# Optimization experiments

Hardware: AMD Instinct MI355X
Metric: run time of the kernel (lower is better)

## Reference

```python
import jax, jax.numpy as jnp
from jax import lax
import numpy as np

WIDTH = 3.0        # tool half-width (voxels)
SIGMA = 1.0        # soft mask edge (voxels)
BLUR_SIGMA = 1.5   # post-deposit isotropic blur sigma (voxels)
EPS = 1e-8


def _gauss_blur(x, sigma):
    """Separable Gaussian blur over the last two axes of x: [B, X, Y]."""
    radius = int(3 * sigma)
    t = jnp.arange(-radius, radius + 1, dtype=x.dtype)
    k = jnp.exp(-0.5 * (t / sigma) ** 2)
    k = k / k.sum()
    x4 = x[:, None]                      # [B,1,X,Y] NCHW
    kh = k.reshape(1, 1, -1, 1)
    x4 = lax.conv_general_dilated(x4, kh, (1, 1), 'SAME')
    kw = k.reshape(1, 1, 1, -1)
    x4 = lax.conv_general_dilated(x4, kw, (1, 1), 'SAME')
    return x4[:, 0]


def setup_inputs() -> dict:
    key = jax.random.key(0)
    k1, k2, k3 = jax.random.split(key, 3)
    B, H, W = 16, 1024, 1024
    occ = jax.random.uniform(k1, (B, H, W), dtype=jnp.float32)
    # push start/end points well inside the grid (voxel coordinates)
    action_start = jax.random.uniform(k2, (B, 3), minval=200.0, maxval=800.0, dtype=jnp.float32)
    action_end = action_start + jax.random.uniform(k3, (B, 3), minval=-150.0, maxval=150.0, dtype=jnp.float32)
    return {"occ": occ, "action_start": action_start, "action_end": action_end}


def reference(occ, action_start, action_end):
    # coordinate-convention transpose (see SplatPushModel docs)
    rho = jnp.swapaxes(occ, 1, 2)            # [B, X, Y]
    B, X, Y = rho.shape
    p0 = action_start[:, :2]                 # [B,2]
    p1 = action_end[:, :2]                   # [B,2]

    d = p1 - p0
    L = jnp.sqrt(jnp.sum(d * d, axis=-1) + EPS)      # [B] segment length
    u = d / L[:, None]                               # unit push direction
    n = jnp.stack([-u[:, 1], u[:, 0]], axis=-1)      # unit normal

    gx = jnp.arange(X, dtype=rho.dtype)[None, :, None]   # [1,X,1]
    gy = jnp.arange(Y, dtype=rho.dtype)[None, None, :]   # [1,1,Y]
    bc = lambda v: v[:, None, None]                      # [B] -> [B,1,1]

    # --- swept band: soft distance-to-segment mask ---
    rx = gx - bc(p0[:, 0])
    ry = gy - bc(p0[:, 1])
    t = jnp.clip(rx * bc(u[:, 0]) + ry * bc(u[:, 1]), 0.0, L[:, None, None])
    dx = rx - t * bc(u[:, 0])
    dy = ry - t * bc(u[:, 1])
    dist = jnp.sqrt(dx * dx + dy * dy + EPS)
    swept = jax.nn.sigmoid((WIDTH - dist) / SIGMA)       # [B,X,Y]

    m_swept = jnp.sum(rho * swept, axis=(1, 2))          # [B] mass to move
    pile_depth = m_swept / (2.0 * WIDTH)                 # [B]

    # --- landing zone probe (rectangle past p1) ---
    qx = gx - bc(p1[:, 0])
    qy = gy - bc(p1[:, 1])
    s = qx * bc(u[:, 0]) + qy * bc(u[:, 1])              # along-direction coord
    r = qx * bc(n[:, 0]) + qy * bc(n[:, 1])              # perpendicular coord
    lat = jax.nn.sigmoid((WIDTH - jnp.abs(r)) / SIGMA)
    probe = jax.nn.sigmoid(s / SIGMA) * jax.nn.sigmoid((bc(pile_depth) - s) / SIGMA) * lat
    existing = jnp.sum(rho * probe, axis=(1, 2))         # [B]
    extra = existing / (2.0 * WIDTH)                     # [B] forward extension

    # --- deposit band, shifted forward by extra_depth ---
    dep_mask = (jax.nn.sigmoid((s - bc(extra)) / SIGMA)
                * jax.nn.sigmoid((bc(extra) + bc(pile_depth) - s) / SIGMA)
                * lat)
    dep_norm = m_swept / (jnp.sum(dep_mask, axis=(1, 2)) + EPS)
    dep = dep_mask * dep_norm[:, None, None]             # mass-conserving deposit

    if BLUR_SIGMA > 0:
        dep = _gauss_blur(dep, BLUR_SIGMA)

    rho_new = rho * (1.0 - swept) + dep
    return jnp.swapaxes(rho_new, 1, 2)
```

## Files before the change

kernel.cpp:

```cpp
#include <hip/hip_runtime.h>
#include <math.h>

#define BB    16
#define HH    1024
#define WW    1024
#define EPSF  1e-8f
#define RAD   4
#define MARG  24.f
#define NB1   128
#define NB3   32
#define WMAX  128
#define FW    (WMAX + 16)
#define UNR   4

struct BlurK { float k[9]; };

__device__ __forceinline__ float sigf(float z) {
    z = fmaxf(fminf(z, 40.f), -40.f);
    return 1.f / (1.f + __expf(-z));
}

struct Geom { float p0x, p0y, p1x, p1y, L, ux, uy; };

__device__ __forceinline__ Geom load_geom(const float* as, const float* ae, int b) {
    Geom g;
    g.p0x = as[3 * b];  g.p0y = as[3 * b + 1];
    g.p1x = ae[3 * b];  g.p1y = ae[3 * b + 1];
    float dx = g.p1x - g.p0x, dy = g.p1y - g.p0y;
    g.L  = sqrtf(dx * dx + dy * dy + EPSF);
    g.ux = dx / g.L;  g.uy = dy / g.L;
    return g;
}

__device__ __forceinline__ float sweptf(const Geom& g, float x, float y) {
    float rx = x - g.p0x, ry = y - g.p0y;
    float t  = fminf(fmaxf(rx * g.ux + ry * g.uy, 0.f), g.L);
    float dx = rx - t * g.ux, dy = ry - t * g.uy;
    float dist = sqrtf(dx * dx + dy * dy + EPSF);
    return sigf(3.f - dist);
}

__device__ __forceinline__ void slat(const Geom& g, float x, float y, float& s, float& lat) {
    float qx = x - g.p1x, qy = y - g.p1y;
    s = qx * g.ux + qy * g.uy;
    float r = qx * (-g.uy) + qy * g.ux;
    lat = sigf(3.f - fabsf(r));
}

__device__ __forceinline__ void capsule_bbox(const Geom& g, float m,
                                             int& x0, int& x1, int& y0, int& y1) {
    x0 = max(0, (int)floorf(fminf(g.p0x, g.p1x) - m));
    x1 = min(WW - 1, (int)ceilf(fmaxf(g.p0x, g.p1x) + m));
    y0 = max(0, (int)floorf(fminf(g.p0y, g.p1y) - m));
    y1 = min(HH - 1, (int)ceilf(fmaxf(g.p0y, g.p1y) + m));
}

__device__ __forceinline__ void strip_bbox(const Geom& g, float s0, float s1, float m,
                                           int& x0, int& x1, int& y0, int& y1) {
    float xmin = 1e9f, xmax = -1e9f, ymin = 1e9f, ymax = -1e9f;
    #pragma unroll
    for (int i = 0; i < 4; i++) {
        float s = (i & 1) ? s1 : s0;
        float r = (i & 2) ? m : -m;
        float x = g.p1x + s * g.ux - r * g.uy;
        float y = g.p1y + s * g.uy + r * g.ux;
        xmin = fminf(xmin, x); xmax = fmaxf(xmax, x);
        ymin = fminf(ymin, y); ymax = fmaxf(ymax, y);
    }
    x0 = max(0, (int)floorf(xmin)); x1 = min(WW - 1, (int)ceilf(xmax));
    y0 = max(0, (int)floorf(ymin)); y1 = min(HH - 1, (int)ceilf(ymax));
}

__device__ __forceinline__ bool ivx(float a, float A, float B, float& lo, float& hi) {
    if (fabsf(a) < 1e-5f) return !(A > 0.f || B < 0.f);
    float l = A / a, h = B / a;
    if (a < 0.f) { float t = l; l = h; h = t; }
    lo = fmaxf(lo, l); hi = fminf(hi, h);
    return true;
}

__device__ __forceinline__ float brb256(float v, float* sm) {
    #pragma unroll
    for (int off = 32; off > 0; off >>= 1) v += __shfl_down(v, off);
    const int lane = threadIdx.x & 63, wid = threadIdx.x >> 6;
    if (lane == 0) sm[wid] = v;
    __syncthreads();
    float r = sm[0] + sm[1] + sm[2] + sm[3];
    __syncthreads();
    return r;
}

__device__ __forceinline__ float brb1024(float v, float* sm) {
    #pragma unroll
    for (int off = 32; off > 0; off >>= 1) v += __shfl_down(v, off);
    const int lane = threadIdx.x & 63, wid = threadIdx.x >> 6;
    if (lane == 0) sm[wid] = v;
    __syncthreads();
    float r = 0.f;
    #pragma unroll
    for (int i = 0; i < 16; i++) r += sm[i];
    __syncthreads();
    return r;
}

__global__ __launch_bounds__(256)
void k_main(const float* __restrict__ occ, const float* __restrict__ as,
            const float* __restrict__ ae, float* __restrict__ out,
            float* __restrict__ part1) {
    const int b = blockIdx.y, bx = blockIdx.x, tid = threadIdx.x;
    Geom g = load_geom(as, ae, b);
    const size_t ibase = (size_t)b << 20;
    const float4* src = (const float4*)(occ + ibase);
    float4*       dst = (float4*)(out + ibase);
    const int yb = bx * 8;
    const int base4 = bx * 2048 + tid;

    float4 v[8];
    #pragma unroll
    for (int k = 0; k < 8; k++) v[k] = src[base4 + k * 256];

    int cx0, cx1, cy0, cy1; capsule_bbox(g, MARG, cx0, cx1, cy0, cy1);
    const int x = tid << 2;
    float msum = 0.f;
    if (x + 3 >= cx0 && x <= cx1) {
        #pragma unroll
        for (int k = 0; k < 8; k++) {
            const int y = yb + k;
            if (y >= cy0 && y <= cy1) {
                const float fy = (float)y, fx = (float)x;
                const float s0 = sweptf(g, fx + 0.f, fy);
                const float s1 = sweptf(g, fx + 1.f, fy);
                const float s2 = sweptf(g, fx + 2.f, fy);
                const float s3 = sweptf(g, fx + 3.f, fy);
                msum += v[k].x * s0 + v[k].y * s1 + v[k].z * s2 + v[k].w * s3;
                v[k].x *= 1.f - s0; v[k].y *= 1.f - s1;
                v[k].z *= 1.f - s2; v[k].w *= 1.f - s3;
            }
        }
    }
    #pragma unroll
    for (int k = 0; k < 8; k++) dst[base4 + k * 256] = v[k];

    __shared__ float sm[4];
    const float bs = brb256(msum, sm);
    if (tid == 0) part1[b * NB1 + bx] = bs;
}

__global__ __launch_bounds__(1024)
void k_probe(const float* __restrict__ occ, const float* __restrict__ as,
             const float* __restrict__ ae, const float* __restrict__ part1,
             float* __restrict__ sc) {
    const int b = blockIdx.x, tid = threadIdx.x;
    const int tx4 = tid & 63;
    const int ty  = tid >> 6;
    __shared__ float sm[16];
    Geom g = load_geom(as, ae, b);
    const float4* src4 = (const float4*)(occ + ((size_t)b << 20));

    const float m_swept = brb1024((tid < NB1) ? part1[b * NB1 + tid] : 0.f, sm);
    const float pile = m_swept * (1.f / 6.f);

    int x0, x1, y0, y1;
    strip_bbox(g, -MARG, pile + MARG, MARG, x0, x1, y0, y1);
    int c0 = x0 >> 2, c1 = x1 >> 2;
    float sum = 0.f;
    for (int cc = c0; cc <= c1; cc += 64) {
        const int c = cc + tx4;
        const bool cok = (c <= c1);
        const float fx = (float)(c << 2);
        for (int y = y0 + ty; y <= y1; y += 16 * UNR) {
            float4 vv[UNR];
            #pragma unroll
            for (int j = 0; j < UNR; j++) {
                const int yy = y + 16 * j;
                vv[j] = (cok && yy <= y1) ? src4[yy * 256 + c]
                                          : make_float4(0.f, 0.f, 0.f, 0.f);
            }
            #pragma unroll
            for (int j = 0; j < UNR; j++) {
                const int yy = y + 16 * j;
                if (cok && yy <= y1) {
                    const float fy = (float)yy;
                    #pragma unroll
                    for (int e = 0; e < 4; e++) {
                        float s, lat; slat(g, fx + (float)e, fy, s, lat);
                        sum += (&vv[j].x)[e] * sigf(s) * sigf(pile - s) * lat;
                    }
                }
            }
        }
    }
    const float existing = brb1024(sum, sm);
    const float extra = existing * (1.f / 6.f);

    strip_bbox(g, extra - MARG, extra + pile + MARG, MARG, x0, x1, y0, y1);
    sum = 0.f;
    {
        const int tx = tid & 127, ty8 = tid >> 7;
        for (int y = y0 + ty8; y <= y1; y += 8) {
            const float fy = (float)y;
            for (int x = x0 + tx; x <= x1; x += 128) {
                float s, lat; slat(g, (float)x, fy, s, lat);
                sum += sigf(s - extra) * sigf(extra + pile - s) * lat;
            }
        }
    }
    const float summask = brb1024(sum, sm);

    if (tid == 0) {
        sc[b * 4 + 0] = pile;
        sc[b * 4 + 1] = extra;
        sc[b * 4 + 2] = m_swept / (summask + EPSF);
    }
}

__global__ __launch_bounds__(256)
void k_dep(const float* __restrict__ as, const float* __restrict__ ae,
           const float* __restrict__ sc, float* __restrict__ out, BlurK wk) {
    const int b = blockIdx.y, bx = blockIdx.x, tid = threadIdx.x;
    const float pile     = sc[b * 4 + 0];
    const float extra    = sc[b * 4 + 1];
    const float dep_norm = sc[b * 4 + 2];
    Geom g = load_geom(as, ae, b);

    int sx0, sx1, sy0, sy1;
    strip_bbox(g, extra - MARG, extra + pile + MARG, MARG, sx0, sx1, sy0, sy1);
    if (sx0 > sx1 || sy0 > sy1) return;
    float* outb = out + ((size_t)b << 20);

    __shared__ float draw[16][FW];
    __shared__ float hb[16][WMAX];

    const int nty = (sy1 - sy0) / 8 + 1;
    const float sA = extra - MARG, sB = extra + pile + MARG;

    for (int ty = bx; ty < nty; ty += NB3) {
        const int yt = sy0 + ty * 8;

        float xlo = 1e9f, xhi = -1e9f;
        #pragma unroll
        for (int r = 0; r < 16; r++) {
            const float dy = (float)(yt - RAD + r) - g.p1y;
            float lo = -1e9f, hi = 1e9f;
            bool ok = ivx(g.ux, sA - dy * g.uy, sB - dy * g.uy, lo, hi);
            ok = ok && ivx(-g.uy, -MARG - dy * g.ux, MARG - dy * g.ux, lo, hi);
            if (ok && lo <= hi) { xlo = fminf(xlo, lo); xhi = fmaxf(xhi, hi); }
        }
        const int csx0 = max(sx0, (int)floorf(xlo + g.p1x));
        const int csx1 = min(sx1, (int)ceilf(xhi + g.p1x));
        if (csx0 > csx1) continue;

        for (int cx = csx0 & ~3; cx <= csx1; cx += WMAX) {
            const int w = min(WMAX, csx1 - cx + 1);

            for (int i = tid; i < 16 * FW; i += 256) {
                const int ly = i / FW, lx = i - ly * FW;
                if (lx < w + 8) {
                    const int gy = yt - RAD + ly, gx = cx - RAD + lx;
                    float val = 0.f;
                    if ((unsigned)gx < WW && (unsigned)gy < HH) {
                        float s, lat; slat(g, (float)gx, (float)gy, s, lat);
                        val = sigf(s - extra) * sigf(extra + pile - s) * lat * dep_norm;
                    }
                    draw[ly][lx] = val;
                }
            }
            __syncthreads();

            for (int i = tid; i < 16 * WMAX; i += 256) {
                const int ly = i >> 7, lx = i & 127;
                if (lx < w) {
                    float acc = 0.f;
                    #pragma unroll
                    for (int j = 0; j < 9; j++) acc += wk.k[j] * draw[ly][lx + j];
                    hb[ly][lx] = acc;
                }
            }
            __syncthreads();

            for (int i = tid; i < 8 * WMAX; i += 256) {
                const int k = i >> 7, lx = i & 127;
                if (lx < w) {
                    float acc = 0.f;
                    #pragma unroll
                    for (int j = 0; j < 9; j++) acc += wk.k[j] * hb[k + j][lx];
                    draw[k][lx] = acc;
                }
            }
            __syncthreads();

            for (int i = tid; i < 8 * WMAX; i += 256) {
                const int k = i >> 7, lx = i & 127;
                const int gy = yt + k, gx = cx + lx;
                if (lx < w && (unsigned)gy < HH && (unsigned)gx < WW)
                    outb[((size_t)gy << 10) + gx] += draw[k][lx];
            }
            __syncthreads();
        }
    }
}

extern "C" void kernel_launch(void* const* d_in, const int* in_sizes, int n_in,
                              void* d_out, int out_size, void* d_ws, size_t ws_size,
                              hipStream_t stream) {
    const float* occ = (const float*)d_in[0];
    const float* as  = (const float*)d_in[1];
    const float* ae  = (const float*)d_in[2];
    float* out   = (float*)d_out;
    float* part1 = (float*)d_ws;
    float* sc    = part1 + BB * NB1;

    BlurK wk;
    {
        float s = 0.f;
        for (int i = 0; i < 9; i++) {
            float t = (float)(i - RAD) / 1.5f;
            wk.k[i] = expf(-0.5f * t * t);
            s += wk.k[i];
        }
        for (int i = 0; i < 9; i++) wk.k[i] /= s;
    }

    k_main <<<dim3(NB1, BB), 256,  0, stream>>>(occ, as, ae, out, part1);
    k_probe<<<dim3(BB),      1024, 0, stream>>>(occ, as, ae, part1, sc);
    k_dep  <<<dim3(NB3, BB), 256,  0, stream>>>(as, ae, sc, out, wk);
}
```

Measured before the change: 158.8 us.

## Split per-batch probe kernel into multi-block existing and summask reductions

```diff
diff --git a/kernel.cpp b/kernel.cpp
--- a/kernel.cpp
+++ b/kernel.cpp
@@ -8,10 +8,10 @@
 #define RAD   4
 #define MARG  24.f
 #define NB1   128
+#define NB2   64
 #define NB3   32
 #define WMAX  128
 #define FW    (WMAX + 16)
-#define UNR   4
 
 struct BlurK { float k[9]; };
 
@@ -86,19 +86,6 @@
     if (lane == 0) sm[wid] = v;
     __syncthreads();
     float r = sm[0] + sm[1] + sm[2] + sm[3];
-    __syncthreads();
-    return r;
-}
-
-__device__ __forceinline__ float brb1024(float v, float* sm) {
-    #pragma unroll
-    for (int off = 32; off > 0; off >>= 1) v += __shfl_down(v, off);
-    const int lane = threadIdx.x & 63, wid = threadIdx.x >> 6;
-    if (lane == 0) sm[wid] = v;
-    __syncthreads();
-    float r = 0.f;
-    #pragma unroll
-    for (int i = 0; i < 16; i++) r += sm[i];
     __syncthreads();
     return r;
 }
@@ -146,83 +133,70 @@
     if (tid == 0) part1[b * NB1 + bx] = bs;
 }
 
-__global__ __launch_bounds__(1024)
-void k_probe(const float* __restrict__ occ, const float* __restrict__ as,
-             const float* __restrict__ ae, const float* __restrict__ part1,
-             float* __restrict__ sc) {
-    const int b = blockIdx.x, tid = threadIdx.x;
-    const int tx4 = tid & 63;
-    const int ty  = tid >> 6;
-    __shared__ float sm[16];
+__global__ __launch_bounds__(256)
+void k_existing(const float* __restrict__ occ, const float* __restrict__ as,
+                const float* __restrict__ ae, const float* __restrict__ part1,
+                float* __restrict__ part2) {
+    const int b = blockIdx.y, bx = blockIdx.x, tid = threadIdx.x;
+    __shared__ float sm[4];
+    const float m_swept = brb256((tid < NB1) ? part1[b * NB1 + tid] : 0.f, sm);
+    const float pile = m_swept * (1.f / 6.f);
+
     Geom g = load_geom(as, ae, b);
-    const float4* src4 = (const float4*)(occ + ((size_t)b << 20));
-
-    const float m_swept = brb1024((tid < NB1) ? part1[b * NB1 + tid] : 0.f, sm);
-    const float pile = m_swept * (1.f / 6.f);
-
+    int x0, x1, y0, y1; strip_bbox(g, -MARG, pile + MARG, MARG, x0, x1, y0, y1);
+    const float* base = occ + ((size_t)b << 20);
+    float sum = 0.f;
+    for (int y = y0 + bx; y <= y1; y += NB2) {
+        const float fy = (float)y;
+        for (int x = x0 + tid; x <= x1; x += 256) {
+            float s, lat; slat(g, (float)x, fy, s, lat);
+            sum += base[((size_t)y << 10) + x] * sigf(s) * sigf(pile - s) * lat;
+        }
+    }
+    const float bs = brb256(sum, sm);
+    if (tid == 0) part2[b * NB2 + bx] = bs;
+}
+
+__global__ __launch_bounds__(256)
+void k_summask(const float* __restrict__ as, const float* __restrict__ ae,
+               const float* __restrict__ part1, const float* __restrict__ part2,
+               float* __restrict__ part3) {
+    const int b = blockIdx.y, bx = blockIdx.x, tid = threadIdx.x;
+    __shared__ float sm[4];
+    const float m_swept  = brb256((tid < NB1) ? part1[b * NB1 + tid] : 0.f, sm);
+    const float existing = brb256((tid < NB2) ? part2[b * NB2 + tid] : 0.f, sm);
+    const float pile  = m_swept * (1.f / 6.f);
+    const float extra = existing * (1.f / 6.f);
+
+    Geom g = load_geom(as, ae, b);
     int x0, x1, y0, y1;
-    strip_bbox(g, -MARG, pile + MARG, MARG, x0, x1, y0, y1);
-    int c0 = x0 >> 2, c1 = x1 >> 2;
+    strip_bbox(g, extra - MARG, extra + pile + MARG, MARG, x0, x1, y0, y1);
     float sum = 0.f;
-    for (int cc = c0; cc <= c1; cc += 64) {
-        const int c = cc + tx4;
-        const bool cok = (c <= c1);
-        const float fx = (float)(c << 2);
-        for (int y = y0 + ty; y <= y1; y += 16 * UNR) {
-            float4 vv[UNR];
-            #pragma unroll
-            for (int j = 0; j < UNR; j++) {
-                const int yy = y + 16 * j;
-                vv[j] = (cok && yy <= y1) ? src4[yy * 256 + c]
-                                          : make_float4(0.f, 0.f, 0.f, 0.f);
-            }
-            #pragma unroll
-            for (int j = 0; j < UNR; j++) {
-                const int yy = y + 16 * j;
-                if (cok && yy <= y1) {
-                    const float fy = (float)yy;
-                    #pragma unroll
-                    for (int e = 0; e < 4; e++) {
-                        float s, lat; slat(g, fx + (float)e, fy, s, lat);
-                        sum += (&vv[j].x)[e] * sigf(s) * sigf(pile - s) * lat;
-                    }
-                }
-            }
-        }
-    }
-    const float existing = brb1024(sum, sm);
-    const float extra = existing * (1.f / 6.f);
-
-    strip_bbox(g, extra - MARG, extra + pile + MARG, MARG, x0, x1, y0, y1);
-    sum = 0.f;
-    {
-        const int tx = tid & 127, ty8 = tid >> 7;
-        for (int y = y0 + ty8; y <= y1; y += 8) {
-            const float fy = (float)y;
-            for (int x = x0 + tx; x <= x1; x += 128) {
-                float s, lat; slat(g, (float)x, fy, s, lat);
-                sum += sigf(s - extra) * sigf(extra + pile - s) * lat;
-            }
-        }
-    }
-    const float summask = brb1024(sum, sm);
-
-    if (tid == 0) {
-        sc[b * 4 + 0] = pile;
-        sc[b * 4 + 1] = extra;
-        sc[b * 4 + 2] = m_swept / (summask + EPSF);
-    }
+    for (int y = y0 + bx; y <= y1; y += NB2) {
+        const float fy = (float)y;
+        for (int x = x0 + tid; x <= x1; x += 256) {
+            float s, lat; slat(g, (float)x, fy, s, lat);
+            sum += sigf(s - extra) * sigf(extra + pile - s) * lat;
+        }
+    }
+    const float bs = brb256(sum, sm);
+    if (tid == 0) part3[b * NB2 + bx] = bs;
 }
 
 __global__ __launch_bounds__(256)
 void k_dep(const float* __restrict__ as, const float* __restrict__ ae,
-           const float* __restrict__ sc, float* __restrict__ out, BlurK wk) {
+           const float* __restrict__ part1, const float* __restrict__ part2,
+           const float* __restrict__ part3, float* __restrict__ out, BlurK wk) {
     const int b = blockIdx.y, bx = blockIdx.x, tid = threadIdx.x;
-    const float pile     = sc[b * 4 + 0];
-    const float extra    = sc[b * 4 + 1];
-    const float dep_norm = sc[b * 4 + 2];
+    __shared__ float sm[4];
+    const float m_swept  = brb256((tid < NB1) ? part1[b * NB1 + tid] : 0.f, sm);
+    const float existing = brb256((tid < NB2) ? part2[b * NB2 + tid] : 0.f, sm);
+    const float summask  = brb256((tid < NB2) ? part3[b * NB2 + tid] : 0.f, sm);
+    const float pile     = m_swept * (1.f / 6.f);
+    const float extra    = existing * (1.f / 6.f);
+    const float dep_norm = m_swept / (summask + EPSF);
+
     Geom g = load_geom(as, ae, b);
-
     int sx0, sx1, sy0, sy1;
     strip_bbox(g, extra - MARG, extra + pile + MARG, MARG, sx0, sx1, sy0, sy1);
     if (sx0 > sx1 || sy0 > sy1) return;
@@ -308,7 +282,8 @@
     const float* ae  = (const float*)d_in[2];
     float* out   = (float*)d_out;
     float* part1 = (float*)d_ws;
-    float* sc    = part1 + BB * NB1;
+    float* part2 = part1 + BB * NB1;
+    float* part3 = part2 + BB * NB2;
 
     BlurK wk;
     {
@@ -321,7 +296,8 @@
         for (int i = 0; i < 9; i++) wk.k[i] /= s;
     }
 
-    k_main <<<dim3(NB1, BB), 256,  0, stream>>>(occ, as, ae, out, part1);
-    k_probe<<<dim3(BB),      1024, 0, stream>>>(occ, as, ae, part1, sc);
-    k_dep  <<<dim3(NB3, BB), 256,  0, stream>>>(as, ae, sc, out, wk);
-}
+    k_main    <<<dim3(NB1, BB), 256, 0, stream>>>(occ, as, ae, out, part1);
+    k_existing<<<dim3(NB2, BB), 256, 0, stream>>>(occ, as, ae, part1, part2);
+    k_summask <<<dim3(NB2, BB), 256, 0, stream>>>(as, ae, part1, part2, part3);
+    k_dep     <<<dim3(NB3, BB), 256, 0, stream>>>(as, ae, part1, part2, part3, out, wk);
+}
```

Result: faster. 136.3 us, median of 2 (-14.2%).
